# Performance work log

Hardware: AMD Instinct MI355X
Metric: run time of the kernel (lower is better)

## Reference

```python
import jax, jax.numpy as jnp
import numpy as np

N = 4096          # nodes per graph
F_IN = 256        # node_feature_dim
D_OUT = 128       # out_dim
E = N * N // 2    # edges per graph (so E1+E2 == N*N, required by .view(N, N))
NEG_SLOPE = 0.2   # PyG GATConv default negative_slope


def setup_inputs() -> dict:
    key = jax.random.key(0)
    k = jax.random.split(key, 7)
    x1 = jax.random.normal(k[0], (N, F_IN), dtype=jnp.float32)
    x2 = jax.random.normal(k[1], (N, F_IN), dtype=jnp.float32)
    edge_index1 = jax.random.randint(k[2], (2, E), 0, N, dtype=jnp.int64)
    edge_index2 = jax.random.randint(k[3], (2, E), 0, N, dtype=jnp.int64)
    W = jax.random.normal(k[4], (F_IN, D_OUT), dtype=jnp.float32) * 0.05
    att_src = jax.random.normal(k[5], (D_OUT,), dtype=jnp.float32) * 0.1
    att_dst = jax.random.normal(k[6], (D_OUT,), dtype=jnp.float32) * 0.1
    return {"x1": x1, "x2": x2, "edge_index1": edge_index1,
            "edge_index2": edge_index2, "W": W,
            "att_src": att_src, "att_dst": att_dst}


def reference(x1, x2, edge_index1, edge_index2, W, att_src, att_dst):
    n = x1.shape[0]
    # combine the two graphs into one block-diagonal graph (graph2 node ids shifted)
    x = jnp.concatenate([x1, x2], axis=0)                       # [2N, F]
    ei = jnp.concatenate([edge_index1, edge_index2 + n], axis=1)  # [2, N*N]
    src, dst = ei[0], ei[1]

    # GATConv (heads=1): linear transform then per-node logit halves
    h = x @ W                    # [2N, D]
    a_s = h @ att_src            # [2N]
    a_d = h @ att_dst            # [2N]

    # per-edge attention logits with leaky-relu
    e = jax.nn.leaky_relu(a_s[src] + a_d[dst], NEG_SLOPE)       # [N*N]

    # numerically-stable segment softmax grouped by destination node
    num_seg = 2 * n
    seg_max = jax.ops.segment_max(e, dst, num_segments=num_seg)
    ex = jnp.exp(e - seg_max[dst])
    denom = jax.ops.segment_sum(ex, dst, num_segments=num_seg)
    alpha = ex / denom[dst]                                     # [N*N]

    # forward returns only the attention weights reshaped to [N, N]
    return alpha.reshape(n, n)
```

## Files before the change

### kernel.cpp

```cpp
#include <hip/hip_runtime.h>


#define NNODES 4096
#define NSEG   8192
#define NEG_SLOPE 0.2f
#define EK_TPB 1024
#define EK_QPB 8192

__global__ void k1_wvec(const float* __restrict__ W,
                        const float* __restrict__ att_src,
                        const float* __restrict__ att_dst,
                        float* __restrict__ wvs, float* __restrict__ wvd) {
    int f = threadIdx.x;
    const float* row = W + f * 128;
    float s = 0.f, d = 0.f;
    #pragma unroll 8
    for (int j = 0; j < 128; ++j) {
        float w = row[j];
        s += w * att_src[j];
        d += w * att_dst[j];
    }
    wvs[f] = s; wvd[f] = d;
}

__global__ void k2_logits(const float* __restrict__ x1, const float* __restrict__ x2,
                          const float* __restrict__ wvs, const float* __restrict__ wvd,
                          float* __restrict__ a_s, float* __restrict__ a_d) {
    int wave = blockIdx.x * 4 + (threadIdx.x >> 6);
    int lane = threadIdx.x & 63;
    const float* xrow = (wave < NNODES) ? (x1 + (size_t)wave * 256)
                                        : (x2 + (size_t)(wave - NNODES) * 256);
    float4 xv  = ((const float4*)xrow)[lane];
    float4 wsv = ((const float4*)wvs)[lane];
    float4 wdv = ((const float4*)wvd)[lane];
    float ps = xv.x*wsv.x + xv.y*wsv.y + xv.z*wsv.z + xv.w*wsv.w;
    float pd = xv.x*wdv.x + xv.y*wdv.y + xv.z*wdv.z + xv.w*wdv.w;
    #pragma unroll
    for (int o = 32; o > 0; o >>= 1) {
        ps += __shfl_down(ps, o);
        pd += __shfl_down(pd, o);
    }
    if (lane == 0) { a_s[wave] = ps; a_d[wave] = pd; }
}

__device__ __forceinline__ float lrelu_exp(float e) {
    e = (e > 0.f) ? e : NEG_SLOPE * e;
    return __expf(e);
}

__global__ __launch_bounds__(EK_TPB) void k3_denom(
        const int* __restrict__ ei1, const int* __restrict__ ei2,
        const float* __restrict__ a_s, const float* __restrict__ a_d,
        float* __restrict__ partials, float* __restrict__ out,
        int E1, int g1_blocks) {
    __shared__ float ssum[NNODES];
    __shared__ float las[NNODES];
    int t = threadIdx.x;
    int b = blockIdx.x;
    const int* sp; int qbase, nodeoff, outq;
    if (b < g1_blocks) { sp = ei1; qbase = b * EK_QPB; nodeoff = 0; outq = qbase; }
    else { sp = ei2; qbase = (b - g1_blocks) * EK_QPB; nodeoff = NNODES; outq = E1/4 + qbase; }
    const int4* s4 = (const int4*)sp;
    const int4* d4 = (const int4*)(sp + E1);
    const float* adg = a_d + nodeoff;

    ((float4*)las)[t]  = ((const float4*)(a_s + nodeoff))[t];
    ((float4*)ssum)[t] = make_float4(0.f, 0.f, 0.f, 0.f);
    __syncthreads();

    float4* out4 = (float4*)out;
    #pragma unroll
    for (int k = 0; k < 8; ++k) {
        int q = qbase + (k << 10) + t;
        int4 sv = s4[q];
        int4 dv = d4[q];
        float ad0 = adg[dv.x], ad1 = adg[dv.y], ad2 = adg[dv.z], ad3 = adg[dv.w];
        float e0 = lrelu_exp(las[sv.x] + ad0);
        float e1 = lrelu_exp(las[sv.y] + ad1);
        float e2 = lrelu_exp(las[sv.z] + ad2);
        float e3 = lrelu_exp(las[sv.w] + ad3);
        atomicAdd(&ssum[dv.x], e0);
        atomicAdd(&ssum[dv.y], e1);
        atomicAdd(&ssum[dv.z], e2);
        atomicAdd(&ssum[dv.w], e3);
        out4[outq + (k << 10) + t] = make_float4(e0, e1, e2, e3);
    }
    __syncthreads();
    float* pb = partials + (size_t)b * NNODES;
    ((float4*)pb)[t] = ((float4*)ssum)[t];
}

__global__ void k4a_reduce(const float* __restrict__ partials,
                           float* __restrict__ partials2, int g1_blocks) {
    int tid = blockIdx.x * blockDim.x + threadIdx.x;
    int c  = tid >> 13;
    int sg = tid & (NSEG - 1);
    int bpc = g1_blocks >> 3;
    int b0 = ((sg < NNODES) ? 0 : g1_blocks) + c * bpc;
    int col = sg & (NNODES - 1);
    float s = 0.f;
    for (int j = 0; j < bpc; ++j)
        s += partials[(size_t)(b0 + j) * NNODES + col];
    partials2[tid] = s;
}

__global__ void k4b_inv(const float* __restrict__ partials2,
                        float* __restrict__ inv_denom) {
    int sg = blockIdx.x * blockDim.x + threadIdx.x;
    float s = 0.f;
    #pragma unroll
    for (int c = 0; c < 8; ++c) s += partials2[c * NSEG + sg];
    inv_denom[sg] = 1.0f / s;
}

__global__ __launch_bounds__(EK_TPB) void k5_alpha(
        const int* __restrict__ ei1, const int* __restrict__ ei2,
        const float* __restrict__ inv_denom,
        float* __restrict__ out, int E1, int g1_blocks) {
    __shared__ float linv[NNODES];
    int t = threadIdx.x;
    int b = blockIdx.x;
    const int* sp; int qbase, nodeoff, outq;
    if (b < g1_blocks) { sp = ei1; qbase = b * EK_QPB; nodeoff = 0; outq = qbase; }
    else { sp = ei2; qbase = (b - g1_blocks) * EK_QPB; nodeoff = NNODES; outq = E1/4 + qbase; }
    const int4* d4 = (const int4*)(sp + E1);

    ((float4*)linv)[t] = ((const float4*)(inv_denom + nodeoff))[t];
    __syncthreads();

    float4* out4 = (float4*)out;
    #pragma unroll
    for (int k = 0; k < 8; ++k) {
        int q = qbase + (k << 10) + t;
        int4  dv = d4[q];
        float4 ex = out4[outq + (k << 10) + t];
        ex.x *= linv[dv.x];
        ex.y *= linv[dv.y];
        ex.z *= linv[dv.z];
        ex.w *= linv[dv.w];
        out4[outq + (k << 10) + t] = ex;
    }
}

extern "C" void kernel_launch(void* const* d_in, const int* in_sizes, int n_in,
                              void* d_out, int out_size, void* d_ws, size_t ws_size,
                              hipStream_t stream) {
    const float* x1      = (const float*)d_in[0];
    const float* x2      = (const float*)d_in[1];
    const int*   ei1     = (const int*)d_in[2];
    const int*   ei2     = (const int*)d_in[3];
    const float* W       = (const float*)d_in[4];
    const float* att_src = (const float*)d_in[5];
    const float* att_dst = (const float*)d_in[6];
    float* out = (float*)d_out;

    const int E1 = in_sizes[2] / 2;

    float* wsf       = (float*)d_ws;
    float* wvs       = wsf;
    float* wvd       = wsf + 256;
    float* a_s       = wsf + 512;
    float* a_d       = wsf + 512 + NSEG;
    float* inv_denom = wsf + 512 + 2*NSEG;
    float* partials2 = wsf + 32768;
    float* partials  = wsf + 131072;

    hipLaunchKernelGGL(k1_wvec, dim3(1), dim3(256), 0, stream,
                       W, att_src, att_dst, wvs, wvd);
    hipLaunchKernelGGL(k2_logits, dim3(2 * NNODES / 4), dim3(256), 0, stream,
                       x1, x2, wvs, wvd, a_s, a_d);

    int g1b = (E1 / 4) / EK_QPB;
    hipLaunchKernelGGL(k3_denom, dim3(2 * g1b), dim3(EK_TPB), 0, stream,
                       ei1, ei2, a_s, a_d, partials, out, E1, g1b);
    hipLaunchKernelGGL(k4a_reduce, dim3(8 * NSEG / 256), dim3(256), 0, stream,
                       partials, partials2, g1b);
    hipLaunchKernelGGL(k4b_inv, dim3(NSEG / 256), dim3(256), 0, stream,
                       partials2, inv_denom);
    hipLaunchKernelGGL(k5_alpha, dim3(2 * g1b), dim3(EK_TPB), 0, stream,
                       ei1, ei2, inv_denom, out, E1, g1b);
}
```

Before: 271.1 us.

## Recompute edge exponentials in alpha pass instead of storing and rereading them

The denominator kernel no longer writes per-edge exponentials to the output. The alpha kernel rereads source indices and recomputes leaky-relu/exp, then scales by the inverse denominator. This removes one full read and one full write of the output buffer in exchange for rereading source indices and redoing the exp. The destination logits are also staged into LDS instead of gathered from global memory, which raises LDS use per block.

```diff
diff --git a/kernel.cpp b/kernel.cpp
--- a/kernel.cpp
+++ b/kernel.cpp
@@ -48,42 +48,39 @@
     return __expf(e);
 }
 
-__global__ __launch_bounds__(EK_TPB) void k3_denom(
+__global__ __launch_bounds__(EK_TPB) void kA_denom(
         const int* __restrict__ ei1, const int* __restrict__ ei2,
         const float* __restrict__ a_s, const float* __restrict__ a_d,
-        float* __restrict__ partials, float* __restrict__ out,
-        int E1, int g1_blocks) {
+        float* __restrict__ partials, int E1, int g1_blocks) {
+    __shared__ float las[NNODES];
+    __shared__ float lad[NNODES];
     __shared__ float ssum[NNODES];
-    __shared__ float las[NNODES];
     int t = threadIdx.x;
     int b = blockIdx.x;
-    const int* sp; int qbase, nodeoff, outq;
-    if (b < g1_blocks) { sp = ei1; qbase = b * EK_QPB; nodeoff = 0; outq = qbase; }
-    else { sp = ei2; qbase = (b - g1_blocks) * EK_QPB; nodeoff = NNODES; outq = E1/4 + qbase; }
+    const int* sp; int qbase, nodeoff;
+    if (b < g1_blocks) { sp = ei1; qbase = b * EK_QPB; nodeoff = 0; }
+    else { sp = ei2; qbase = (b - g1_blocks) * EK_QPB; nodeoff = NNODES; }
     const int4* s4 = (const int4*)sp;
     const int4* d4 = (const int4*)(sp + E1);
-    const float* adg = a_d + nodeoff;
 
     ((float4*)las)[t]  = ((const float4*)(a_s + nodeoff))[t];
+    ((float4*)lad)[t]  = ((const float4*)(a_d + nodeoff))[t];
     ((float4*)ssum)[t] = make_float4(0.f, 0.f, 0.f, 0.f);
     __syncthreads();
 
-    float4* out4 = (float4*)out;
     #pragma unroll
     for (int k = 0; k < 8; ++k) {
         int q = qbase + (k << 10) + t;
         int4 sv = s4[q];
         int4 dv = d4[q];
-        float ad0 = adg[dv.x], ad1 = adg[dv.y], ad2 = adg[dv.z], ad3 = adg[dv.w];
-        float e0 = lrelu_exp(las[sv.x] + ad0);
-        float e1 = lrelu_exp(las[sv.y] + ad1);
-        float e2 = lrelu_exp(las[sv.z] + ad2);
-        float e3 = lrelu_exp(las[sv.w] + ad3);
+        float e0 = lrelu_exp(las[sv.x] + lad[dv.x]);
+        float e1 = lrelu_exp(las[sv.y] + lad[dv.y]);
+        float e2 = lrelu_exp(las[sv.z] + lad[dv.z]);
+        float e3 = lrelu_exp(las[sv.w] + lad[dv.w]);
         atomicAdd(&ssum[dv.x], e0);
         atomicAdd(&ssum[dv.y], e1);
         atomicAdd(&ssum[dv.z], e2);
         atomicAdd(&ssum[dv.w], e3);
-        out4[outq + (k << 10) + t] = make_float4(e0, e1, e2, e3);
     }
     __syncthreads();
     float* pb = partials + (size_t)b * NNODES;
@@ -113,18 +110,24 @@
     inv_denom[sg] = 1.0f / s;
 }
 
-__global__ __launch_bounds__(EK_TPB) void k5_alpha(
+__global__ __launch_bounds__(EK_TPB) void kB_alpha(
         const int* __restrict__ ei1, const int* __restrict__ ei2,
+        const float* __restrict__ a_s, const float* __restrict__ a_d,
         const float* __restrict__ inv_denom,
         float* __restrict__ out, int E1, int g1_blocks) {
+    __shared__ float las[NNODES];
+    __shared__ float lad[NNODES];
     __shared__ float linv[NNODES];
     int t = threadIdx.x;
     int b = blockIdx.x;
     const int* sp; int qbase, nodeoff, outq;
     if (b < g1_blocks) { sp = ei1; qbase = b * EK_QPB; nodeoff = 0; outq = qbase; }
     else { sp = ei2; qbase = (b - g1_blocks) * EK_QPB; nodeoff = NNODES; outq = E1/4 + qbase; }
+    const int4* s4 = (const int4*)sp;
     const int4* d4 = (const int4*)(sp + E1);
 
+    ((float4*)las)[t]  = ((const float4*)(a_s + nodeoff))[t];
+    ((float4*)lad)[t]  = ((const float4*)(a_d + nodeoff))[t];
     ((float4*)linv)[t] = ((const float4*)(inv_denom + nodeoff))[t];
     __syncthreads();
 
@@ -132,13 +135,13 @@
     #pragma unroll
     for (int k = 0; k < 8; ++k) {
         int q = qbase + (k << 10) + t;
-        int4  dv = d4[q];
-        float4 ex = out4[outq + (k << 10) + t];
-        ex.x *= linv[dv.x];
-        ex.y *= linv[dv.y];
-        ex.z *= linv[dv.z];
-        ex.w *= linv[dv.w];
-        out4[outq + (k << 10) + t] = ex;
+        int4 sv = s4[q];
+        int4 dv = d4[q];
+        float e0 = lrelu_exp(las[sv.x] + lad[dv.x]) * linv[dv.x];
+        float e1 = lrelu_exp(las[sv.y] + lad[dv.y]) * linv[dv.y];
+        float e2 = lrelu_exp(las[sv.z] + lad[dv.z]) * linv[dv.z];
+        float e3 = lrelu_exp(las[sv.w] + lad[dv.w]) * linv[dv.w];
+        out4[outq + (k << 10) + t] = make_float4(e0, e1, e2, e3);
     }
 }
 
@@ -171,12 +174,12 @@
                        x1, x2, wvs, wvd, a_s, a_d);
 
     int g1b = (E1 / 4) / EK_QPB;
-    hipLaunchKernelGGL(k3_denom, dim3(2 * g1b), dim3(EK_TPB), 0, stream,
-                       ei1, ei2, a_s, a_d, partials, out, E1, g1b);
+    hipLaunchKernelGGL(kA_denom, dim3(2 * g1b), dim3(EK_TPB), 0, stream,
+                       ei1, ei2, a_s, a_d, partials, E1, g1b);
     hipLaunchKernelGGL(k4a_reduce, dim3(8 * NSEG / 256), dim3(256), 0, stream,
                        partials, partials2, g1b);
     hipLaunchKernelGGL(k4b_inv, dim3(NSEG / 256), dim3(256), 0, stream,
                        partials2, inv_denom);
-    hipLaunchKernelGGL(k5_alpha, dim3(2 * g1b), dim3(EK_TPB), 0, stream,
-                       ei1, ei2, inv_denom, out, E1, g1b);
+    hipLaunchKernelGGL(kB_alpha, dim3(2 * g1b), dim3(EK_TPB), 0, stream,
+                       ei1, ei2, a_s, a_d, inv_denom, out, E1, g1b);
 }
```

New measurement: 276.5 us. Within noise of the previous version (+2.0%).

## Factor leaky-relu exp into per-node tables to remove per-edge exp

Applied to the files above, without the earlier changes.

Rewrites exp(leaky_relu(a_s+a_d)) as a product of per-node exponentials, choosing the branch by comparing exp(a_s) with exp(-a_d). The per-edge exp and global a_d gathers go away: the edge pass gathers precomputed per-source pairs from LDS, accumulates into two split per-destination sums, and stores a signed unnormalized value. The second pass then scales by per-destination factors that fold in the inverse denominator. This trades transcendental work and a global gather for extra LDS footprint (about 64KB per block, which may reduce occupancy), and it carries some risk of overflow or underflow in exp(a_s) and exp(-a_d) for large logits.

```diff
diff --git a/kernel.cpp b/kernel.cpp
--- a/kernel.cpp
+++ b/kernel.cpp
@@ -25,7 +25,8 @@
 
 __global__ void k2_logits(const float* __restrict__ x1, const float* __restrict__ x2,
                           const float* __restrict__ wvs, const float* __restrict__ wvd,
-                          float* __restrict__ a_s, float* __restrict__ a_d) {
+                          float* __restrict__ a_d, float2* __restrict__ espair,
+                          float* __restrict__ wtab) {
     int wave = blockIdx.x * 4 + (threadIdx.x >> 6);
     int lane = threadIdx.x & 63;
     const float* xrow = (wave < NNODES) ? (x1 + (size_t)wave * 256)
@@ -40,21 +41,22 @@
         ps += __shfl_down(ps, o);
         pd += __shfl_down(pd, o);
     }
-    if (lane == 0) { a_s[wave] = ps; a_d[wave] = pd; }
-}
-
-__device__ __forceinline__ float lrelu_exp(float e) {
-    e = (e > 0.f) ? e : NEG_SLOPE * e;
-    return __expf(e);
-}
-
-__global__ __launch_bounds__(EK_TPB) void k3_denom(
+    if (lane == 0) {
+        a_d[wave]    = pd;
+        espair[wave] = make_float2(__expf(ps), __expf(NEG_SLOPE * ps));
+        wtab[wave]   = __expf(-pd);
+    }
+}
+
+__global__ __launch_bounds__(EK_TPB) void kA_denom(
         const int* __restrict__ ei1, const int* __restrict__ ei2,
-        const float* __restrict__ a_s, const float* __restrict__ a_d,
+        const float2* __restrict__ espair, const float* __restrict__ wtab,
+        const float* __restrict__ a_d,
         float* __restrict__ partials, float* __restrict__ out,
         int E1, int g1_blocks) {
-    __shared__ float ssum[NNODES];
-    __shared__ float las[NNODES];
+    __shared__ float2 les[NNODES];
+    __shared__ float  lw[NNODES];
+    __shared__ float  s12[2 * NNODES];
     int t = threadIdx.x;
     int b = blockIdx.x;
     const int* sp; int qbase, nodeoff, outq;
@@ -62,10 +64,16 @@
     else { sp = ei2; qbase = (b - g1_blocks) * EK_QPB; nodeoff = NNODES; outq = E1/4 + qbase; }
     const int4* s4 = (const int4*)sp;
     const int4* d4 = (const int4*)(sp + E1);
-    const float* adg = a_d + nodeoff;
-
-    ((float4*)las)[t]  = ((const float4*)(a_s + nodeoff))[t];
-    ((float4*)ssum)[t] = make_float4(0.f, 0.f, 0.f, 0.f);
+
+    {
+        float4* lesv = (float4*)les;
+        const float4* gesv = (const float4*)(espair + nodeoff);
+        lesv[t] = gesv[t]; lesv[t + 1024] = gesv[t + 1024];
+        ((float4*)lw)[t] = ((const float4*)(wtab + nodeoff))[t];
+        float4* sv = (float4*)s12;
+        sv[t] = make_float4(0.f,0.f,0.f,0.f);
+        sv[t + 1024] = make_float4(0.f,0.f,0.f,0.f);
+    }
     __syncthreads();
 
     float4* out4 = (float4*)out;
@@ -74,20 +82,28 @@
         int q = qbase + (k << 10) + t;
         int4 sv = s4[q];
         int4 dv = d4[q];
-        float ad0 = adg[dv.x], ad1 = adg[dv.y], ad2 = adg[dv.z], ad3 = adg[dv.w];
-        float e0 = lrelu_exp(las[sv.x] + ad0);
-        float e1 = lrelu_exp(las[sv.y] + ad1);
-        float e2 = lrelu_exp(las[sv.z] + ad2);
-        float e3 = lrelu_exp(las[sv.w] + ad3);
-        atomicAdd(&ssum[dv.x], e0);
-        atomicAdd(&ssum[dv.y], e1);
-        atomicAdd(&ssum[dv.z], e2);
-        atomicAdd(&ssum[dv.w], e3);
-        out4[outq + (k << 10) + t] = make_float4(e0, e1, e2, e3);
+        float2 e0 = les[sv.x], e1 = les[sv.y], e2 = les[sv.z], e3 = les[sv.w];
+        float  w0 = lw[dv.x],  w1 = lw[dv.y],  w2 = lw[dv.z],  w3 = lw[dv.w];
+        bool p0 = e0.x > w0, p1 = e1.x > w1, p2 = e2.x > w2, p3 = e3.x > w3;
+        atomicAdd(&s12[dv.x + (p0 ? 0 : NNODES)], p0 ? e0.x : e0.y);
+        atomicAdd(&s12[dv.y + (p1 ? 0 : NNODES)], p1 ? e1.x : e1.y);
+        atomicAdd(&s12[dv.z + (p2 ? 0 : NNODES)], p2 ? e2.x : e2.y);
+        atomicAdd(&s12[dv.w + (p3 ? 0 : NNODES)], p3 ? e3.x : e3.y);
+        out4[outq + (k << 10) + t] = make_float4(p0 ? e0.x : -e0.y,
+                                                 p1 ? e1.x : -e1.y,
+                                                 p2 ? e2.x : -e2.y,
+                                                 p3 ? e3.x : -e3.y);
     }
     __syncthreads();
-    float* pb = partials + (size_t)b * NNODES;
-    ((float4*)pb)[t] = ((float4*)ssum)[t];
+
+    float4 ad4 = ((const float4*)(a_d + nodeoff))[t];
+    int n = 4 * t;
+    float4 r;
+    r.x = __expf(ad4.x) * s12[n+0] + __expf(NEG_SLOPE * ad4.x) * s12[n+0+NNODES];
+    r.y = __expf(ad4.y) * s12[n+1] + __expf(NEG_SLOPE * ad4.y) * s12[n+1+NNODES];
+    r.z = __expf(ad4.z) * s12[n+2] + __expf(NEG_SLOPE * ad4.z) * s12[n+2+NNODES];
+    r.w = __expf(ad4.w) * s12[n+3] + __expf(NEG_SLOPE * ad4.w) * s12[n+3+NNODES];
+    ((float4*)(partials + (size_t)b * NNODES))[t] = r;
 }
 
 __global__ void k4a_reduce(const float* __restrict__ partials,
@@ -105,40 +121,47 @@
 }
 
 __global__ void k4b_inv(const float* __restrict__ partials2,
-                        float* __restrict__ inv_denom) {
+                        const float* __restrict__ a_d,
+                        float2* __restrict__ uv) {
     int sg = blockIdx.x * blockDim.x + threadIdx.x;
     float s = 0.f;
     #pragma unroll
     for (int c = 0; c < 8; ++c) s += partials2[c * NSEG + sg];
-    inv_denom[sg] = 1.0f / s;
-}
-
-__global__ __launch_bounds__(EK_TPB) void k5_alpha(
+    float inv = 1.0f / s;
+    float ad = a_d[sg];
+    uv[sg] = make_float2(__expf(ad) * inv, __expf(NEG_SLOPE * ad) * inv);
+}
+
+__global__ __launch_bounds__(EK_TPB) void kB_alpha(
         const int* __restrict__ ei1, const int* __restrict__ ei2,
-        const float* __restrict__ inv_denom,
+        const float2* __restrict__ uv,
         float* __restrict__ out, int E1, int g1_blocks) {
-    __shared__ float linv[NNODES];
+    __shared__ float2 luv[NNODES];
     int t = threadIdx.x;
     int b = blockIdx.x;
-    const int* sp; int qbase, nodeoff, outq;
-    if (b < g1_blocks) { sp = ei1; qbase = b * EK_QPB; nodeoff = 0; outq = qbase; }
-    else { sp = ei2; qbase = (b - g1_blocks) * EK_QPB; nodeoff = NNODES; outq = E1/4 + qbase; }
+    const int* sp; int qbase, outq;
+    const float2* uvg;
+    if (b < g1_blocks) { sp = ei1; qbase = b * EK_QPB; uvg = uv; outq = qbase; }
+    else { sp = ei2; qbase = (b - g1_blocks) * EK_QPB; uvg = uv + NNODES; outq = E1/4 + qbase; }
     const int4* d4 = (const int4*)(sp + E1);
 
-    ((float4*)linv)[t] = ((const float4*)(inv_denom + nodeoff))[t];
+    float4* luvv = (float4*)luv;
+    const float4* guv = (const float4*)uvg;
+    luvv[t] = guv[t]; luvv[t + 1024] = guv[t + 1024];
     __syncthreads();
 
     float4* out4 = (float4*)out;
     #pragma unroll
     for (int k = 0; k < 8; ++k) {
         int q = qbase + (k << 10) + t;
-        int4  dv = d4[q];
-        float4 ex = out4[outq + (k << 10) + t];
-        ex.x *= linv[dv.x];
-        ex.y *= linv[dv.y];
-        ex.z *= linv[dv.z];
-        ex.w *= linv[dv.w];
-        out4[outq + (k << 10) + t] = ex;
+        int4   dv  = d4[q];
+        float4 val = out4[outq + (k << 10) + t];
+        float2 u0 = luv[dv.x], u1 = luv[dv.y], u2 = luv[dv.z], u3 = luv[dv.w];
+        val.x = (val.x > 0.f) ? val.x * u0.x : (-val.x) * u0.y;
+        val.y = (val.y > 0.f) ? val.y * u1.x : (-val.y) * u1.y;
+        val.z = (val.z > 0.f) ? val.z * u2.x : (-val.z) * u2.y;
+        val.w = (val.w > 0.f) ? val.w * u3.x : (-val.w) * u3.y;
+        out4[outq + (k << 10) + t] = val;
     }
 }
 
@@ -159,24 +182,25 @@
     float* wsf       = (float*)d_ws;
     float* wvs       = wsf;
     float* wvd       = wsf + 256;
-    float* a_s       = wsf + 512;
-    float* a_d       = wsf + 512 + NSEG;
-    float* inv_denom = wsf + 512 + 2*NSEG;
-    float* partials2 = wsf + 32768;
+    float* a_d       = wsf + 512;
+    float2* espair   = (float2*)(wsf + 512 + NSEG);
+    float* wtab      = wsf + 512 + NSEG + 2*NSEG;
+    float2* uv       = (float2*)(wsf + 512 + 4*NSEG);
+    float* partials2 = wsf + 65536;
     float* partials  = wsf + 131072;
 
     hipLaunchKernelGGL(k1_wvec, dim3(1), dim3(256), 0, stream,
                        W, att_src, att_dst, wvs, wvd);
     hipLaunchKernelGGL(k2_logits, dim3(2 * NNODES / 4), dim3(256), 0, stream,
-                       x1, x2, wvs, wvd, a_s, a_d);
+                       x1, x2, wvs, wvd, a_d, espair, wtab);
 
     int g1b = (E1 / 4) / EK_QPB;
-    hipLaunchKernelGGL(k3_denom, dim3(2 * g1b), dim3(EK_TPB), 0, stream,
-                       ei1, ei2, a_s, a_d, partials, out, E1, g1b);
+    hipLaunchKernelGGL(kA_denom, dim3(2 * g1b), dim3(EK_TPB), 0, stream,
+                       ei1, ei2, espair, wtab, a_d, partials, out, E1, g1b);
     hipLaunchKernelGGL(k4a_reduce, dim3(8 * NSEG / 256), dim3(256), 0, stream,
                        partials, partials2, g1b);
     hipLaunchKernelGGL(k4b_inv, dim3(NSEG / 256), dim3(256), 0, stream,
-                       partials2, inv_denom);
-    hipLaunchKernelGGL(k5_alpha, dim3(2 * g1b), dim3(EK_TPB), 0, stream,
-                       ei1, ei2, inv_denom, out, E1, g1b);
-}
+                       partials2, a_d, uv);
+    hipLaunchKernelGGL(kB_alpha, dim3(2 * g1b), dim3(EK_TPB), 0, stream,
+                       ei1, ei2, uv, out, E1, g1b);
+}
```

Result: no change. 274.4 us (+1.2%).
